# Kernel optimization log

Measured on AMD Instinct MI355X. Metric: run time of the kernel, lower is better.

The kernel has to match this reference:

```python
import jax, jax.numpy as jnp
import numpy as np
import math

NUM_BANDS = 8
BINS = 512
CROPSIZE = 1024
BATCH = 4


def _dwconv(x, w, b):
    # depthwise Conv1d, kernel=3, padding=1, groups=C. x: [B,C,W], w: [C,1,3], b: [C]
    y = jax.lax.conv_general_dilated(x, w, window_strides=(1,), padding=((1, 1),),
                                     feature_group_count=x.shape[1])
    return y + b[None, :, None]


def setup_inputs() -> dict:
    key = jax.random.key(0)
    ks = jax.random.split(key, 20)
    s = 0.02
    lin = lambda k: jax.random.normal(k, (BINS, BINS), jnp.float32) * s
    cw = lambda k: jax.random.normal(k, (BINS, 1, 3), jnp.float32) * s
    vec = lambda k: jax.random.normal(k, (BINS,), jnp.float32) * s
    return {
        "x": jax.random.normal(ks[0], (BATCH, CROPSIZE, BINS), jnp.float32),
        "q_w": lin(ks[1]), "q_b": vec(ks[2]), "q_cw": cw(ks[3]), "q_cb": vec(ks[4]),
        "k_w": lin(ks[5]), "k_b": vec(ks[6]), "k_cw": cw(ks[7]), "k_cb": vec(ks[8]),
        "v_w": lin(ks[9]), "v_b": vec(ks[10]), "v_cw": cw(ks[11]), "v_cb": vec(ks[12]),
        "o_w": lin(ks[13]), "o_b": vec(ks[14]),
        "er": jax.random.normal(ks[15], (BINS // NUM_BANDS, CROPSIZE), jnp.float32),
    }


def reference(x, q_w, q_b, q_cw, q_cb, k_w, k_b, k_cw, k_cb,
              v_w, v_b, v_cw, v_cb, o_w, o_b, er):
    b, w, c = x.shape
    h = NUM_BANDS

    def proj(lw, lb, cwt, cbt):
        y = x @ lw.T + lb                                   # [b,w,c] linear
        y = _dwconv(y.transpose(0, 2, 1), cwt, cbt)         # [b,c,w] depthwise conv
        return y.transpose(0, 2, 1).reshape(b, w, h, -1)    # [b,w,h,d]

    q = proj(q_w, q_b, q_cw, q_cb).transpose(0, 2, 1, 3)    # [b,h,w,d]
    k = proj(k_w, k_b, k_cw, k_cb).transpose(0, 2, 3, 1)    # [b,h,d,w]
    v = proj(v_w, v_b, v_cw, v_cb).transpose(0, 2, 1, 3)    # [b,h,w,d]

    # relative position bias via pad/transpose/slice skew
    qe = jnp.einsum('bhwd,dc->bhwc', q, er)                 # [b,h,w,cropsize]
    p = jnp.pad(qe, ((0, 0), (0, 0), (0, 0), (1, 0)))       # [b,h,w,cs+1]
    p = p.transpose(0, 1, 3, 2)[:, :, 1:, :]                # [b,h,cs,w] == [b,h,w,w]

    qk = (q @ k + p) / math.sqrt(c)
    a = jax.nn.softmax(qk, axis=-1)
    out = (a @ v).transpose(0, 2, 1, 3).reshape(b, w, c)    # [b,w,c]
    return out @ o_w.T + o_b
```

## Files before the change

### kernel.cpp

```cpp
#include <hip/hip_runtime.h>
#include <hip/hip_bf16.h>
#include <math.h>


#define CROP 1024
#define NB 512
#define NH 8
#define HD 64
#define NBATCH 4
#define MTOT 4096
#define NBH 32
#define JSPLIT 4
#define ROWS_TOT 32768

typedef __attribute__((ext_vector_type(8))) short bf8;
typedef __attribute__((ext_vector_type(4))) float f4;
typedef __attribute__((ext_vector_type(8))) _Float16 h8;

__device__ __forceinline__ short f2bf(float f) {
  __hip_bfloat16 h = __float2bfloat16(f);
  short s;
  __builtin_memcpy(&s, &h, 2);
  return s;
}
__device__ __forceinline__ float bf2f(short s) {
  union { unsigned u; float f; } v; v.u = ((unsigned)(unsigned short)s) << 16;
  return v.f;
}
__device__ __forceinline__ f4 mfma16(bf8 a, bf8 b, f4 c) {
  return __builtin_amdgcn_mfma_f32_16x16x32_bf16(a, b, c, 0, 0, 0);
}
__device__ __forceinline__ float fast_exp2(float x) {
#if __has_builtin(__builtin_amdgcn_exp2f)
  return __builtin_amdgcn_exp2f(x);
#else
  float r;
  asm("v_exp_f32 %0, %1" : "=v"(r) : "v"(x));
  return r;
#endif
}

#define ISC 0.044194173824159216f
#define QSCALE 0.06376743237228177f

__global__ __launch_bounds__(256) void prep_kernel(
    const float* __restrict__ x,
    const float* __restrict__ w0, const float* __restrict__ w1,
    const float* __restrict__ w2, const float* __restrict__ w3,
    const float* __restrict__ er,
    short* __restrict__ xb, short* __restrict__ wb, short* __restrict__ erT)
{
  const int blk = blockIdx.x;
  const int t = threadIdx.x;
  if (blk < 1024) {
    int i = (blk * 256 + t) * 8;
    f4 a = *(const f4*)(x + i);
    f4 b = *(const f4*)(x + i + 4);
    bf8 o;
#pragma unroll
    for (int j = 0; j < 4; ++j) { o[j] = f2bf(a[j]); o[4 + j] = f2bf(b[j]); }
    *(bf8*)(xb + i) = o;
  } else if (blk < 1536) {
    int p = (blk - 1024) >> 7;
    const float* s = (p == 0) ? w0 : (p == 1) ? w1 : (p == 2) ? w2 : w3;
    int i = (((blk - 1024) & 127) * 256 + t) * 8;
    f4 a = *(const f4*)(s + i);
    f4 b = *(const f4*)(s + i + 4);
    bf8 o;
#pragma unroll
    for (int j = 0; j < 4; ++j) { o[j] = f2bf(a[j]); o[4 + j] = f2bf(b[j]); }
    *(bf8*)(wb + (size_t)p * NB * NB + i) = o;
  } else {
    int idx = (blk - 1536) * 256 + t;
    int w = idx >> 6, d = idx & 63;
    erT[idx] = f2bf(er[d * CROP + w]);
  }
}

__global__ __launch_bounds__(256) void proj_gemm2(
    const short* __restrict__ Xb, const short* __restrict__ Wb,
    const float* __restrict__ B0, const float* __restrict__ B1, const float* __restrict__ B2,
    short* __restrict__ O0, short* __restrict__ O1, short* __restrict__ O2)
{
  const int p = blockIdx.z;
  const short* Wt = Wb + (size_t)p * NB * NB;
  const float* Bb = (p == 0) ? B0 : (p == 1) ? B1 : B2;
  short* Out = (p == 0) ? O0 : (p == 1) ? O1 : O2;

  __shared__ short As[64][72];
  __shared__ short Bs[64][72];

  const int t = threadIdx.x;
  const int lane = t & 63, wave = t >> 6;
  const int wr = wave >> 1, wc = wave & 1;
  const int l15 = lane & 15, l4 = lane >> 4;
  const int bm = blockIdx.x, bn = blockIdx.y;

  f4 acc[2][2];
#pragma unroll
  for (int i = 0; i < 2; ++i)
#pragma unroll
    for (int j = 0; j < 2; ++j) acc[i][j] = (f4){0.f, 0.f, 0.f, 0.f};

  const int sr = t >> 2, sc = (t & 3) * 16;
  const short* xrow = Xb + (size_t)(bm * 64 + sr) * NB + sc;
  const short* wrow = Wt + (size_t)(bn * 64 + sr) * NB + sc;

  for (int k0 = 0; k0 < NB; k0 += 64) {
    bf8 a0 = *(const bf8*)(xrow + k0);
    bf8 a1 = *(const bf8*)(xrow + k0 + 8);
    bf8 b0 = *(const bf8*)(wrow + k0);
    bf8 b1 = *(const bf8*)(wrow + k0 + 8);
    __syncthreads();
    *(bf8*)&As[sr][sc] = a0;
    *(bf8*)&As[sr][sc + 8] = a1;
    *(bf8*)&Bs[sr][sc] = b0;
    *(bf8*)&Bs[sr][sc + 8] = b1;
    __syncthreads();
#pragma unroll
    for (int ks = 0; ks < 2; ++ks) {
      bf8 af[2], bg[2];
#pragma unroll
      for (int mt = 0; mt < 2; ++mt)
        af[mt] = *(bf8*)&As[wr * 32 + mt * 16 + l15][ks * 32 + l4 * 8];
#pragma unroll
      for (int nt = 0; nt < 2; ++nt)
        bg[nt] = *(bf8*)&Bs[wc * 32 + nt * 16 + l15][ks * 32 + l4 * 8];
#pragma unroll
      for (int mt = 0; mt < 2; ++mt)
#pragma unroll
        for (int nt = 0; nt < 2; ++nt)
          acc[mt][nt] = mfma16(af[mt], bg[nt], acc[mt][nt]);
    }
  }
#pragma unroll
  for (int mt = 0; mt < 2; ++mt)
#pragma unroll
    for (int nt = 0; nt < 2; ++nt)
#pragma unroll
      for (int r = 0; r < 4; ++r) {
        int row = bm * 64 + wr * 32 + mt * 16 + l4 * 4 + r;
        int col = bn * 64 + wc * 32 + nt * 16 + l15;
        Out[(size_t)row * NB + col] = f2bf(acc[mt][nt][r] + Bb[col]);
      }
}

__global__ __launch_bounds__(256) void dwconv_all(
    const short* __restrict__ q0p, const short* __restrict__ k0p,
    const short* __restrict__ v0p,
    const float* __restrict__ qcw, const float* __restrict__ qcb,
    const float* __restrict__ kcw, const float* __restrict__ kcb,
    const float* __restrict__ vcw, const float* __restrict__ vcb,
    short* __restrict__ qb, short* __restrict__ kb, short* __restrict__ vb)
{
  const int blk = blockIdx.x;
  const int t = threadIdx.x;

  if (blk < 2048) {
    const int p = blk >> 10;
    const short* src = p ? k0p : q0p;
    const float* cw = p ? kcw : qcw;
    const float* cb = p ? kcb : qcb;
    short* dst = p ? kb : qb;
    const float scale = p ? 1.0f : QSCALE;

    const int idx = ((blk & 1023) * 256 + t) * 8;
    const int c = idx & (NB - 1);
    const int m = idx >> 9;
    const int w = m & (CROP - 1);
    const int b = m >> 10;

    const bf8 z = (bf8){0, 0, 0, 0, 0, 0, 0, 0};
    bf8 mid = *(const bf8*)(src + idx);
    bf8 lo = (w > 0) ? *(const bf8*)(src + idx - NB) : z;
    bf8 hi = (w < CROP - 1) ? *(const bf8*)(src + idx + NB) : z;

    f4 cwv[6];
#pragma unroll
    for (int i = 0; i < 6; ++i) cwv[i] = *(const f4*)(cw + c * 3 + i * 4);
    f4 cb0 = *(const f4*)(cb + c);
    f4 cb1 = *(const f4*)(cb + c + 4);

    bf8 o;
#pragma unroll
    for (int j = 0; j < 8; ++j) {
      float k0w = cwv[(3 * j) >> 2][(3 * j) & 3];
      float k1w = cwv[(3 * j + 1) >> 2][(3 * j + 1) & 3];
      float k2w = cwv[(3 * j + 2) >> 2][(3 * j + 2) & 3];
      float bias = (j < 4) ? cb0[j] : cb1[j - 4];
      float acc = bias + k0w * bf2f(lo[j]) + k1w * bf2f(mid[j]) + k2w * bf2f(hi[j]);
      o[j] = f2bf(acc * scale);
    }
    const int h = c >> 6, d0 = c & 63;
    *(bf8*)(dst + ((size_t)(b * NH + h) * CROP + w) * HD + d0) = o;
  } else {
    __shared__ short S[66][72];
    const int blk2 = blk - 2048;
    const int w0 = (blk2 & 15) * 64, c0 = ((blk2 >> 4) & 7) * 64, b = blk2 >> 7;

#pragma unroll
    for (int i = 0; i < 3; ++i) {
      int r = i * 32 + (t >> 3);
      if (r < 66) {
        int w = w0 - 1 + r;
        int cg = (t & 7) * 8;
        bf8 val = (bf8){0, 0, 0, 0, 0, 0, 0, 0};
        if (w >= 0 && w < CROP)
          val = *(const bf8*)(v0p + ((size_t)b * CROP + w) * NB + c0 + cg);
        *(bf8*)&S[r][cg] = val;
      }
    }
    __syncthreads();

    const int c = t & 63, wv = t >> 6;
    const float k0w = vcw[(c0 + c) * 3 + 0];
    const float k1w = vcw[(c0 + c) * 3 + 1];
    const float k2w = vcw[(c0 + c) * 3 + 2];
    const float bias = vcb[c0 + c];

    float xa = bf2f(S[wv * 16][c]);
    float xb2 = bf2f(S[wv * 16 + 1][c]);
    short res[16];
#pragma unroll
    for (int ww = 0; ww < 16; ++ww) {
      float xc = bf2f(S[wv * 16 + ww + 2][c]);
      res[ww] = f2bf(bias + k0w * xa + k1w * xb2 + k2w * xc);
      xa = xb2; xb2 = xc;
    }
    short* dst = vb + ((size_t)(b * NB) + c0 + c) * CROP + w0 + wv * 16;
    *(bf8*)dst = *(bf8*)&res[0];
    *(bf8*)(dst + 8) = *(bf8*)&res[8];
  }
}

__global__ __launch_bounds__(512) void attn_part(
    const short* __restrict__ Qb, const short* __restrict__ Kb,
    const short* __restrict__ Vb, const short* __restrict__ ErT,
    _Float16* __restrict__ Op, float* __restrict__ lbuf)
{
  __shared__ short Ks[64][72];
  __shared__ short Qs[64][72];
  __shared__ short Vs[64][72];
  __shared__ short Ps[8][16][72];

  const int qt = blockIdx.x, bh = blockIdx.y, s = blockIdx.z;
  const int t = threadIdx.x;
  const int lane = t & 63, wave = t >> 6;
  const int l15 = lane & 15, l4 = lane >> 4;
  const int wq = qt * 128 + wave * 16;

  bf8 qa[2], ea[2];
  {
    const short* qrow = Qb + ((size_t)bh * CROP + wq + l15) * HD + l4 * 8;
    qa[0] = *(const bf8*)(qrow);
    qa[1] = *(const bf8*)(qrow + 32);
    const short* erow = ErT + (size_t)(wq + l15) * HD + l4 * 8;
    ea[0] = *(const bf8*)(erow);
    ea[1] = *(const bf8*)(erow + 32);
  }

  float lsum[4] = {0.f, 0.f, 0.f, 0.f};
  f4 oacc[4];
#pragma unroll
  for (int nt = 0; nt < 4; ++nt) oacc[nt] = (f4){0.f, 0.f, 0.f, 0.f};

  const int sr2 = t >> 3, sc2 = (t & 7) * 8;
  const short* ksrc = Kb + ((size_t)bh * CROP + sr2) * HD + sc2;
  const short* qsrc = Qb + ((size_t)bh * CROP + sr2) * HD + sc2;
  const short* vsrc = Vb + ((size_t)bh * HD + sr2) * CROP + sc2;

  const int jbase = s * (CROP / JSPLIT);
  const int JLEN = CROP / JSPLIT;

  bf8 rk = *(const bf8*)(ksrc + jbase * HD);
  bf8 rq = *(const bf8*)(qsrc + jbase * HD);
  bf8 rv = *(const bf8*)(vsrc + jbase);

  for (int jj = 0; jj < JLEN; jj += 64) {
    __syncthreads();
    *(bf8*)&Ks[sr2][sc2] = rk;
    *(bf8*)&Qs[sr2][sc2] = rq;
    *(bf8*)&Vs[sr2][sc2] = rv;
    __syncthreads();

    const int jn = jj + 64;
    if (jn < JLEN) {
      rk = *(const bf8*)(ksrc + (jbase + jn) * HD);
      rq = *(const bf8*)(qsrc + (jbase + jn) * HD);
      rv = *(const bf8*)(vsrc + jbase + jn);
    }

    f4 sacc[4];
#pragma unroll
    for (int nt = 0; nt < 4; ++nt) sacc[nt] = (f4){0.f, 0.f, 0.f, 0.f};
    __builtin_amdgcn_s_setprio(1);
#pragma unroll
    for (int ks = 0; ks < 2; ++ks) {
#pragma unroll
      for (int nt = 0; nt < 4; ++nt) {
        bf8 kf = *(bf8*)&Ks[nt * 16 + l15][ks * 32 + l4 * 8];
        sacc[nt] = mfma16(qa[ks], kf, sacc[nt]);
        bf8 qf = *(bf8*)&Qs[nt * 16 + l15][ks * 32 + l4 * 8];
        sacc[nt] = mfma16(ea[ks], qf, sacc[nt]);
      }
    }
    __builtin_amdgcn_s_setprio(0);

#pragma unroll
    for (int r = 0; r < 4; ++r) {
      const int prow = l4 * 4 + r;
      float pv0 = fast_exp2(sacc[0][r]);
      float pv1 = fast_exp2(sacc[1][r]);
      float pv2 = fast_exp2(sacc[2][r]);
      float pv3 = fast_exp2(sacc[3][r]);
      lsum[r] += (pv0 + pv1) + (pv2 + pv3);
      Ps[wave][prow][0 * 16 + l15] = f2bf(pv0);
      Ps[wave][prow][1 * 16 + l15] = f2bf(pv1);
      Ps[wave][prow][2 * 16 + l15] = f2bf(pv2);
      Ps[wave][prow][3 * 16 + l15] = f2bf(pv3);
    }

    __builtin_amdgcn_s_setprio(1);
#pragma unroll
    for (int ks = 0; ks < 2; ++ks) {
      bf8 pf = *(bf8*)&Ps[wave][l15][ks * 32 + l4 * 8];
#pragma unroll
      for (int nt = 0; nt < 4; ++nt) {
        bf8 vf = *(bf8*)&Vs[nt * 16 + l15][ks * 32 + l4 * 8];
        oacc[nt] = mfma16(pf, vf, oacc[nt]);
      }
    }
    __builtin_amdgcn_s_setprio(0);
  }

#pragma unroll
  for (int r = 0; r < 4; ++r) {
#pragma unroll
    for (int off = 1; off < 16; off <<= 1)
      lsum[r] += __shfl_xor(lsum[r], off);
  }

#pragma unroll
  for (int r = 0; r < 4; ++r) {
    const int row = wq + l4 * 4 + r;
    const size_t ridx = (size_t)(s * NBH + bh) * CROP + row;
#pragma unroll
    for (int nt = 0; nt < 4; ++nt)
      Op[ridx * HD + nt * 16 + l15] = (_Float16)oacc[nt][r];
    if (l15 == 0) lbuf[ridx] = lsum[r];
  }
}

__global__ __launch_bounds__(256) void attn_combine(
    const _Float16* __restrict__ Op, const float* __restrict__ lbuf,
    short* __restrict__ Ao)
{
  const int t = threadIdx.x;
  const int idx = blockIdx.x * 32 + (t >> 3);
  const int dth = (t & 7) * 8;
  float l = 0.f;
#pragma unroll
  for (int s = 0; s < JSPLIT; ++s) l += lbuf[(size_t)s * ROWS_TOT + idx];
  float inv = 1.f / l;
  float o[8] = {0, 0, 0, 0, 0, 0, 0, 0};
#pragma unroll
  for (int s = 0; s < JSPLIT; ++s) {
    h8 v = *(const h8*)(Op + ((size_t)s * ROWS_TOT + idx) * HD + dth);
#pragma unroll
    for (int j = 0; j < 8; ++j) o[j] += (float)v[j];
  }
  const int bh = idx >> 10, row = idx & (CROP - 1);
  const int b = bh >> 3, h = bh & 7;
  short* dst = Ao + ((size_t)(b * CROP + row)) * NB + h * HD + dth;
  bf8 ov;
#pragma unroll
  for (int j = 0; j < 8; ++j) ov[j] = f2bf(o[j] * inv);
  *(bf8*)dst = ov;
}

__global__ __launch_bounds__(256) void out_gemm2(
    const short* __restrict__ A, const short* __restrict__ Wt,
    const float* __restrict__ Bb, float* __restrict__ Out)
{
  __shared__ short As[64][72];
  __shared__ short Bs[64][72];
  const int t = threadIdx.x;
  const int lane = t & 63, wave = t >> 6;
  const int wr = wave >> 1, wc = wave & 1;
  const int l15 = lane & 15, l4 = lane >> 4;
  const int bm = blockIdx.x, bn = blockIdx.y;

  f4 acc[2][2];
#pragma unroll
  for (int i = 0; i < 2; ++i)
#pragma unroll
    for (int j = 0; j < 2; ++j) acc[i][j] = (f4){0.f, 0.f, 0.f, 0.f};

  const int sr = t >> 2, sc = (t & 3) * 16;
  const short* arow = A + (size_t)(bm * 64 + sr) * NB + sc;
  const short* wrow = Wt + (size_t)(bn * 64 + sr) * NB + sc;

  for (int k0 = 0; k0 < NB; k0 += 64) {
    bf8 a0 = *(const bf8*)(arow + k0);
    bf8 a1 = *(const bf8*)(arow + k0 + 8);
    bf8 b0 = *(const bf8*)(wrow + k0);
    bf8 b1 = *(const bf8*)(wrow + k0 + 8);
    __syncthreads();
    *(bf8*)&As[sr][sc] = a0;
    *(bf8*)&As[sr][sc + 8] = a1;
    *(bf8*)&Bs[sr][sc] = b0;
    *(bf8*)&Bs[sr][sc + 8] = b1;
    __syncthreads();
#pragma unroll
    for (int ks = 0; ks < 2; ++ks) {
      bf8 af[2], bg[2];
#pragma unroll
      for (int mt = 0; mt < 2; ++mt)
        af[mt] = *(bf8*)&As[wr * 32 + mt * 16 + l15][ks * 32 + l4 * 8];
#pragma unroll
      for (int nt = 0; nt < 2; ++nt)
        bg[nt] = *(bf8*)&Bs[wc * 32 + nt * 16 + l15][ks * 32 + l4 * 8];
#pragma unroll
      for (int mt = 0; mt < 2; ++mt)
#pragma unroll
        for (int nt = 0; nt < 2; ++nt)
          acc[mt][nt] = mfma16(af[mt], bg[nt], acc[mt][nt]);
    }
  }
#pragma unroll
  for (int mt = 0; mt < 2; ++mt)
#pragma unroll
    for (int nt = 0; nt < 2; ++nt)
#pragma unroll
      for (int r = 0; r < 4; ++r) {
        int row = bm * 64 + wr * 32 + mt * 16 + l4 * 4 + r;
        int col = bn * 64 + wc * 32 + nt * 16 + l15;
        Out[(size_t)row * NB + col] = acc[mt][nt][r] + Bb[col];
      }
}

extern "C" void kernel_launch(void* const* d_in, const int* in_sizes, int n_in,
                              void* d_out, int out_size, void* d_ws, size_t ws_size,
                              hipStream_t stream) {
  (void)in_sizes; (void)n_in; (void)out_size; (void)ws_size;
  const float* x    = (const float*)d_in[0];
  const float* q_w  = (const float*)d_in[1];
  const float* q_b  = (const float*)d_in[2];
  const float* q_cw = (const float*)d_in[3];
  const float* q_cb = (const float*)d_in[4];
  const float* k_w  = (const float*)d_in[5];
  const float* k_b  = (const float*)d_in[6];
  const float* k_cw = (const float*)d_in[7];
  const float* k_cb = (const float*)d_in[8];
  const float* v_w  = (const float*)d_in[9];
  const float* v_b  = (const float*)d_in[10];
  const float* v_cw = (const float*)d_in[11];
  const float* v_cb = (const float*)d_in[12];
  const float* o_w  = (const float*)d_in[13];
  const float* o_b  = (const float*)d_in[14];
  const float* er   = (const float*)d_in[15];
  float* out = (float*)d_out;

  char* ws = (char*)d_ws;
  const size_t MB = 1u << 20;
  short* q0  = (short*)(ws + 0 * MB);
  short* k0  = (short*)(ws + 4 * MB);
  short* v0  = (short*)(ws + 8 * MB);
  short* qb2 = (short*)(ws + 12 * MB);
  short* kb2 = (short*)(ws + 16 * MB);
  short* vb2 = (short*)(ws + 20 * MB);
  short* ao  = (short*)(ws + 24 * MB);
  short* erT = (short*)(ws + 28 * MB);
  short* xb  = (short*)(ws + 29 * MB);
  short* wb  = (short*)(ws + 33 * MB);
  _Float16* Op = (_Float16*)(ws + 36 * MB);
  float* lbuf  = (float*)(ws + 52 * MB);

  prep_kernel<<<dim3(1792), dim3(256), 0, stream>>>(
      x, q_w, k_w, v_w, o_w, er, xb, wb, erT);
  proj_gemm2<<<dim3(64, 8, 3), dim3(256), 0, stream>>>(
      xb, wb, q_b, k_b, v_b, q0, k0, v0);
  dwconv_all<<<dim3(2560), dim3(256), 0, stream>>>(
      q0, k0, v0, q_cw, q_cb, k_cw, k_cb, v_cw, v_cb, qb2, kb2, vb2);
  attn_part<<<dim3(8, NBH, JSPLIT), dim3(512), 0, stream>>>(
      qb2, kb2, vb2, erT, Op, lbuf);
  attn_combine<<<dim3(1024), dim3(256), 0, stream>>>(Op, lbuf, ao);
  out_gemm2<<<dim3(64, 8), dim3(256), 0, stream>>>(
      ao, wb + 3 * NB * NB, o_b, out);
}
```

Before: 71.16 us.

## Use 128x128 tiles with direct global-to-LDS loads in projection GEMM; drop Q LDS staging

The QKV projection GEMM is rewritten to use 128x128 output tiles over a fused 1536-column weight matrix, 4x4 MFMA tiles per wave, and global_load_lds staging into XOR-swizzled LDS. This is meant to raise data reuse and avoid LDS bank conflicts and register round-trips. Separately, the attention kernel no longer stages the Q tile (used for the relative-position term) through LDS and reads it straight from global memory, trading LDS traffic and space for uncoalesced global or L2 reads. The swizzle has to match how global_load_lds places each lane's 16 bytes. If that builtin is missing, a per-lane fallback store is used instead.

```diff
diff --git a/kernel.cpp b/kernel.cpp
--- a/kernel.cpp
+++ b/kernel.cpp
@@ -40,6 +40,16 @@
 #endif
 }
 
+__device__ __forceinline__ void stage16(const short* g, short* ldsbase, int lane) {
+#if __has_builtin(__builtin_amdgcn_global_load_lds)
+  __builtin_amdgcn_global_load_lds(
+      (const __attribute__((address_space(1))) void*)g,
+      (__attribute__((address_space(3))) void*)ldsbase, 16, 0, 0);
+#else
+  *(bf8*)(ldsbase + lane * 8) = *(const bf8*)g;
+#endif
+}
+
 #define ISC 0.044194173824159216f
 #define QSCALE 0.06376743237228177f
 
@@ -77,72 +87,89 @@
   }
 }
 
-__global__ __launch_bounds__(256) void proj_gemm2(
+__device__ __forceinline__ void gemm128_loop(
+    const short* __restrict__ A, const short* __restrict__ Bm,
+    short* As, short* Bs, int rowA0, int rowB0, f4 (&acc)[4][4], int t)
+{
+  const int lane = t & 63, wave = t >> 6;
+  const int wr = wave >> 1, wc = wave & 1;
+  const int l15 = lane & 15, l4 = lane >> 4;
+  const int crow = lane >> 3;
+  const int csub = lane & 7;
+  const int kb = (csub * 16) ^ (crow << 4);
+
+  for (int k0 = 0; k0 < NB; k0 += 64) {
+    __syncthreads();
+#pragma unroll
+    for (int i = 0; i < 4; ++i) {
+      const int c = wave * 4 + i;
+      stage16(A + (size_t)(rowA0 + c * 8 + crow) * NB + k0 + (kb >> 1),
+              As + c * 512, lane);
+      stage16(Bm + (size_t)(rowB0 + c * 8 + crow) * NB + k0 + (kb >> 1),
+              Bs + c * 512, lane);
+    }
+    __syncthreads();
+#pragma unroll
+    for (int ks = 0; ks < 2; ++ks) {
+      bf8 af[4], bg[4];
+#pragma unroll
+      for (int mt = 0; mt < 4; ++mt) {
+        const int row = wr * 64 + mt * 16 + l15;
+        const int byt = (ks * 64 + l4 * 16) ^ ((row & 7) << 4);
+        af[mt] = *(const bf8*)&As[row * 64 + (byt >> 1)];
+      }
+#pragma unroll
+      for (int nt = 0; nt < 4; ++nt) {
+        const int row = wc * 64 + nt * 16 + l15;
+        const int byt = (ks * 64 + l4 * 16) ^ ((row & 7) << 4);
+        bg[nt] = *(const bf8*)&Bs[row * 64 + (byt >> 1)];
+      }
+#pragma unroll
+      for (int mt = 0; mt < 4; ++mt)
+#pragma unroll
+        for (int nt = 0; nt < 4; ++nt)
+          acc[mt][nt] = mfma16(af[mt], bg[nt], acc[mt][nt]);
+    }
+  }
+}
+
+__global__ __launch_bounds__(256) void proj_gemm3(
     const short* __restrict__ Xb, const short* __restrict__ Wb,
     const float* __restrict__ B0, const float* __restrict__ B1, const float* __restrict__ B2,
     short* __restrict__ O0, short* __restrict__ O1, short* __restrict__ O2)
 {
-  const int p = blockIdx.z;
-  const short* Wt = Wb + (size_t)p * NB * NB;
+  __shared__ short As[128 * 64];
+  __shared__ short Bs[128 * 64];
+  f4 acc[4][4];
+#pragma unroll
+  for (int i = 0; i < 4; ++i)
+#pragma unroll
+    for (int j = 0; j < 4; ++j) acc[i][j] = (f4){0.f, 0.f, 0.f, 0.f};
+
+  const int bm = blockIdx.x, bn = blockIdx.y;
+  gemm128_loop(Xb, Wb, As, Bs, bm * 128, bn * 128, acc, threadIdx.x);
+
+  const int p = bn >> 2;
   const float* Bb = (p == 0) ? B0 : (p == 1) ? B1 : B2;
   short* Out = (p == 0) ? O0 : (p == 1) ? O1 : O2;
-
-  __shared__ short As[64][72];
-  __shared__ short Bs[64][72];
+  const int ncol0 = (bn & 3) * 128;
 
   const int t = threadIdx.x;
   const int lane = t & 63, wave = t >> 6;
   const int wr = wave >> 1, wc = wave & 1;
   const int l15 = lane & 15, l4 = lane >> 4;
-  const int bm = blockIdx.x, bn = blockIdx.y;
-
-  f4 acc[2][2];
-#pragma unroll
-  for (int i = 0; i < 2; ++i)
-#pragma unroll
-    for (int j = 0; j < 2; ++j) acc[i][j] = (f4){0.f, 0.f, 0.f, 0.f};
-
-  const int sr = t >> 2, sc = (t & 3) * 16;
-  const short* xrow = Xb + (size_t)(bm * 64 + sr) * NB + sc;
-  const short* wrow = Wt + (size_t)(bn * 64 + sr) * NB + sc;
-
-  for (int k0 = 0; k0 < NB; k0 += 64) {
-    bf8 a0 = *(const bf8*)(xrow + k0);
-    bf8 a1 = *(const bf8*)(xrow + k0 + 8);
-    bf8 b0 = *(const bf8*)(wrow + k0);
-    bf8 b1 = *(const bf8*)(wrow + k0 + 8);
-    __syncthreads();
-    *(bf8*)&As[sr][sc] = a0;
-    *(bf8*)&As[sr][sc + 8] = a1;
-    *(bf8*)&Bs[sr][sc] = b0;
-    *(bf8*)&Bs[sr][sc + 8] = b1;
-    __syncthreads();
-#pragma unroll
-    for (int ks = 0; ks < 2; ++ks) {
-      bf8 af[2], bg[2];
-#pragma unroll
-      for (int mt = 0; mt < 2; ++mt)
-        af[mt] = *(bf8*)&As[wr * 32 + mt * 16 + l15][ks * 32 + l4 * 8];
-#pragma unroll
-      for (int nt = 0; nt < 2; ++nt)
-        bg[nt] = *(bf8*)&Bs[wc * 32 + nt * 16 + l15][ks * 32 + l4 * 8];
-#pragma unroll
-      for (int mt = 0; mt < 2; ++mt)
-#pragma unroll
-        for (int nt = 0; nt < 2; ++nt)
-          acc[mt][nt] = mfma16(af[mt], bg[nt], acc[mt][nt]);
-    }
-  }
-#pragma unroll
-  for (int mt = 0; mt < 2; ++mt)
-#pragma unroll
-    for (int nt = 0; nt < 2; ++nt)
+#pragma unroll
+  for (int mt = 0; mt < 4; ++mt)
+#pragma unroll
+    for (int nt = 0; nt < 4; ++nt) {
+      const int col = ncol0 + wc * 64 + nt * 16 + l15;
+      const float bias = Bb[col];
 #pragma unroll
       for (int r = 0; r < 4; ++r) {
-        int row = bm * 64 + wr * 32 + mt * 16 + l4 * 4 + r;
-        int col = bn * 64 + wc * 32 + nt * 16 + l15;
-        Out[(size_t)row * NB + col] = f2bf(acc[mt][nt][r] + Bb[col]);
-      }
+        const int row = bm * 128 + wr * 64 + mt * 16 + l4 * 4 + r;
+        Out[(size_t)row * NB + col] = f2bf(acc[mt][nt][r] + bias);
+      }
+    }
 }
 
 __global__ __launch_bounds__(256) void dwconv_all(
@@ -239,7 +266,6 @@
     _Float16* __restrict__ Op, float* __restrict__ lbuf)
 {
   __shared__ short Ks[64][72];
-  __shared__ short Qs[64][72];
   __shared__ short Vs[64][72];
   __shared__ short Ps[8][16][72];
 
@@ -266,27 +292,25 @@
 
   const int sr2 = t >> 3, sc2 = (t & 7) * 8;
   const short* ksrc = Kb + ((size_t)bh * CROP + sr2) * HD + sc2;
-  const short* qsrc = Qb + ((size_t)bh * CROP + sr2) * HD + sc2;
   const short* vsrc = Vb + ((size_t)bh * HD + sr2) * CROP + sc2;
+  const short* qjbase = Qb + ((size_t)bh * CROP + l15) * HD + l4 * 8;
 
   const int jbase = s * (CROP / JSPLIT);
   const int JLEN = CROP / JSPLIT;
 
   bf8 rk = *(const bf8*)(ksrc + jbase * HD);
-  bf8 rq = *(const bf8*)(qsrc + jbase * HD);
   bf8 rv = *(const bf8*)(vsrc + jbase);
 
   for (int jj = 0; jj < JLEN; jj += 64) {
+    const int j0 = jbase + jj;
     __syncthreads();
     *(bf8*)&Ks[sr2][sc2] = rk;
-    *(bf8*)&Qs[sr2][sc2] = rq;
     *(bf8*)&Vs[sr2][sc2] = rv;
     __syncthreads();
 
     const int jn = jj + 64;
     if (jn < JLEN) {
       rk = *(const bf8*)(ksrc + (jbase + jn) * HD);
-      rq = *(const bf8*)(qsrc + (jbase + jn) * HD);
       rv = *(const bf8*)(vsrc + jbase + jn);
     }
 
@@ -300,7 +324,7 @@
       for (int nt = 0; nt < 4; ++nt) {
         bf8 kf = *(bf8*)&Ks[nt * 16 + l15][ks * 32 + l4 * 8];
         sacc[nt] = mfma16(qa[ks], kf, sacc[nt]);
-        bf8 qf = *(bf8*)&Qs[nt * 16 + l15][ks * 32 + l4 * 8];
+        bf8 qf = *(const bf8*)(qjbase + (size_t)(j0 + nt * 16) * HD + ks * 32);
         sacc[nt] = mfma16(ea[ks], qf, sacc[nt]);
       }
     }
@@ -478,7 +502,7 @@
 
   prep_kernel<<<dim3(1792), dim3(256), 0, stream>>>(
       x, q_w, k_w, v_w, o_w, er, xb, wb, erT);
-  proj_gemm2<<<dim3(64, 8, 3), dim3(256), 0, stream>>>(
+  proj_gemm3<<<dim3(32, 12), dim3(256), 0, stream>>>(
       xb, wb, q_b, k_b, v_b, q0, k0, v0);
   dwconv_all<<<dim3(2560), dim3(256), 0, stream>>>(
       q0, k0, v0, q_cw, q_cb, k_cw, k_cb, v_cw, v_cb, qb2, kb2, vb2);
```

Measured after the change: 89.46 us. 1.26x slower.
